# Kernel optimization log

Measured on AMD Instinct MI355X. Metric: run time of the kernel, lower is better.

Reference implementation:

```python
import jax, jax.numpy as jnp
import numpy as np

BSZ, SL, D, K, K_U, K_Y, SCALE = 4, 2048, 256, 24, 3, 2, 4
H = SCALE * D


def _hankel(n):
    i = np.arange(1, n + 1, dtype=np.float64)
    s = i[:, None] + i[None, :]
    return 2.0 / (s ** 3 - s)


def setup_inputs() -> dict:
    key = jax.random.key(0)
    ks = jax.random.split(key, 9)
    Z = _hankel(SL)
    ev, evec = np.linalg.eigh(Z)  # ascending
    sigma = jnp.asarray(np.clip(ev[-K:], 1e-12, None), jnp.float32)  # (K,)
    phi = jnp.asarray(evec[:, -K:], jnp.float32)  # (SL, K) top-k eigenvectors
    s = 0.02
    return {
        'x': jax.random.normal(ks[0], (BSZ, SL, D), jnp.float32),
        'sigma': sigma,
        'phi': phi,
        'rms_w': jnp.ones((D,), jnp.float32),
        'M_u': jax.random.normal(ks[1], (K_U, D, D), jnp.float32) * s,
        'M_phi_plus': jax.random.normal(ks[2], (K, D, D), jnp.float32) * s,
        'M_phi_minus': jax.random.normal(ks[3], (K, D, D), jnp.float32) * s,
        'm_y': jax.random.normal(ks[4], (K_Y, D, D), jnp.float32) * s,
        'w1': jax.random.normal(ks[5], (D, H), jnp.float32) * s,
        'v': jax.random.normal(ks[6], (D, H), jnp.float32) * s,
        'w2': jax.random.normal(ks[7], (H, D), jnp.float32) * s,
    }


def _rmsnorm(x, w, eps=1e-6):
    return x * jax.lax.rsqrt(jnp.mean(x * x, axis=-1, keepdims=True) + eps) * w


def _shift(u, i):
    # causal time shift: out[:, t] = u[:, t-i], zero-padded
    if i == 0:
        return u
    return jnp.pad(u, ((0, 0), (i, 0), (0, 0)))[:, :-i, :]


def _causal_conv(phi, u):
    # U[b,t,k,d] = sum_{s<=t} phi[s,k] * u[b,t-s,d], via FFT (linear conv, length 2*sl)
    sl = u.shape[1]
    n = 2 * sl
    Fu = jnp.fft.rfft(u, n=n, axis=1)  # (b, nf, d)
    Fp = jnp.fft.rfft(phi, n=n, axis=0)  # (nf, k)
    prod = Fu[:, :, None, :] * Fp[None, :, :, None]  # (b, nf, k, d)
    return jnp.fft.irfft(prod, n=n, axis=1)[:, :sl]  # (b, sl, k, d)


def _stu(u, sigma, phi, M_u, M_phi_plus, M_phi_minus, m_y):
    k_u = M_u.shape[0]
    ar_u = sum(jnp.einsum('btd,od->bto', _shift(u, i), M_u[i]) for i in range(k_u))
    # spectral term: eigenfilter causal convolutions on u and alternating-sign u
    alt = jnp.where(jnp.arange(u.shape[1]) % 2 == 0, 1.0, -1.0)[None, :, None]
    Up = _causal_conv(phi, u)
    Um = _causal_conv(phi, u * alt)
    sr = sigma ** 0.25
    spectral = (jnp.einsum('btkd,k,kod->bto', Up, sr, M_phi_plus)
                + jnp.einsum('btkd,k,kod->bto', Um, sr, M_phi_minus))
    y = ar_u + spectral  # (b, sl, d)
    # sequential AR recurrence over outputs: yhat_t = y_t + sum_i m_y[i] @ yhat_{t-1-i}
    k_y, d = m_y.shape[0], m_y.shape[2]
    b = u.shape[0]

    def step(carry, y_t):  # carry: (k_y, b, d), most recent first
        ar = jnp.einsum('kod,kbd->bo', m_y, carry)
        yhat = y_t + ar
        carry = jnp.concatenate([yhat[None], carry[:-1]], axis=0)
        return carry, ar

    carry0 = jnp.zeros((k_y, b, d), u.dtype)
    _, ar_y = jax.lax.scan(step, carry0, jnp.swapaxes(y, 0, 1))
    return y + jnp.swapaxes(ar_y, 0, 1)


def reference(x, sigma, phi, rms_w, M_u, M_phi_plus, M_phi_minus, m_y, w1, v, w2):
    z = x
    h = _stu(_rmsnorm(x, rms_w), sigma, phi, M_u, M_phi_plus, M_phi_minus, m_y)
    mlp = (jax.nn.silu(h @ w1) * (h @ v)) @ w2  # SwiGLU
    h = h + mlp
    return h + z
```

## Files before the change

kernel.cpp:

```cpp
#include <hip/hip_runtime.h>
#include <hip/hip_bf16.h>
#include <math.h>

#define SLEN 2048
#define DIM 256
#define NB 4
#define NKF 24
#define NH 1024
#define NROW (NB*SLEN)
#define NTOT (NB*SLEN*DIM)

#define BM 128
#define BN 256
#define BKK 32
#define PADK 40

#define KG 3
#define KPB 8
#define VELEMS ((size_t)NKF*NB*DIM*SLEN)

typedef __attribute__((ext_vector_type(8))) short bf16x8;
typedef __attribute__((ext_vector_type(4))) float f32x4;

struct __align__(16) U4 { unsigned int a, b, c, d; };
struct __align__(8)  S4 { unsigned short x, y, z, w; };

__device__ __forceinline__ unsigned short f2b(float v){
    union { __hip_bfloat16 h; unsigned short u; } cv;
    cv.h = __float2bfloat16(v);
    return cv.u;
}
__device__ __forceinline__ float b2f(unsigned short s){
    union { __hip_bfloat16 h; unsigned short u; } cv;
    cv.u = s;
    return __bfloat162float(cv.h);
}

__device__ __forceinline__ void gl_lds(const unsigned short* g, unsigned short* l){
    __builtin_amdgcn_global_load_lds((const __attribute__((address_space(1))) void*)g,
                                     (__attribute__((address_space(3))) void*)l, 16, 0, 0);
}

__device__ __forceinline__ int swzS(int row, int g){
    return ((row >> 3) << 5) + (g << 3) + ((row & 7) ^ g);
}

__global__ void k_prep(const float4* __restrict__ Mu, const float4* __restrict__ Mp,
                       const float4* __restrict__ Mm,
                       const float* __restrict__ w1, const float* __restrict__ vv,
                       const float* __restrict__ w2, const float* __restrict__ my,
                       const float* __restrict__ phi,
                       S4* __restrict__ MuB, S4* __restrict__ MpB, S4* __restrict__ MmB,
                       unsigned short* __restrict__ w1T, unsigned short* __restrict__ vT,
                       unsigned short* __restrict__ w2T,
                       unsigned short* __restrict__ pw, unsigned short* __restrict__ pwTs,
                       unsigned short* __restrict__ Q, unsigned short* __restrict__ Tt){
    int bid = blockIdx.x, tix = threadIdx.x;
    if (bid < 192){
        int i = bid*256 + tix;
        float4 v = Mu[i];
        S4 p; p.x=f2b(v.x); p.y=f2b(v.y); p.z=f2b(v.z); p.w=f2b(v.w);
        MuB[i] = p; return;
    }
    bid -= 192;
    if (bid < 1536){
        int i = bid*256 + tix;
        float4 v = Mp[i];
        S4 p; p.x=f2b(v.x); p.y=f2b(v.y); p.z=f2b(v.z); p.w=f2b(v.w);
        MpB[i] = p; return;
    }
    bid -= 1536;
    if (bid < 1536){
        int i = bid*256 + tix;
        float4 v = Mm[i];
        S4 p; p.x=f2b(v.x); p.y=f2b(v.y); p.z=f2b(v.z); p.w=f2b(v.w);
        MmB[i] = p; return;
    }
    bid -= 1536;
    if (bid < 1024){
        int i = bid*256 + tix; int r = i >> 10, c = i & 1023;
        w1T[(size_t)c*DIM + r] = f2b(w1[i]); return;
    }
    bid -= 1024;
    if (bid < 1024){
        int i = bid*256 + tix; int r = i >> 10, c = i & 1023;
        vT[(size_t)c*DIM + r] = f2b(vv[i]); return;
    }
    bid -= 1024;
    if (bid < 1024){
        int i = bid*256 + tix; int r = i >> 8, c = i & 255;
        w2T[(size_t)c*NH + r] = f2b(w2[i]); return;
    }
    bid -= 1024;
    if (bid < 1024){
        int i = bid*256 + tix;
        int r = i >> 9, c = i & 511;
        float v;
        if (r < 256) v = (c < 256) ? my[r*256 + c] : my[256*256 + r*256 + (c - 256)];
        else         v = (c == r - 256) ? 1.0f : 0.0f;
        unsigned short bb = f2b(v);
        pw [262144 + (size_t)r*512 + c] = bb;
        pwTs[(size_t)c*512 + r] = bb;
        if (r < 256 && c < 256) Q[65536 + r*256 + c] = bb;
        return;
    }
    bid -= 1024;
    {
        int i = bid*256 + tix;
        int e   = (i & 7) * 4;
        int row = (i >> 3) & 127;
        int c   = (i >> 10) & 7;
        int rem = (i >> 13) & 15;
        int k   = i >> 17;
        int d0 = rem*128 + row - (c*32 + e);
        S4 p;
        p.x = (d0   >= 0) ? f2b(phi[(size_t)(d0  )*NKF + k]) : (unsigned short)0;
        p.y = (d0-1 >= 0) ? f2b(phi[(size_t)(d0-1)*NKF + k]) : (unsigned short)0;
        p.z = (d0-2 >= 0) ? f2b(phi[(size_t)(d0-2)*NKF + k]) : (unsigned short)0;
        p.w = (d0-3 >= 0) ? f2b(phi[(size_t)(d0-3)*NKF + k]) : (unsigned short)0;
        size_t base = ((size_t)((k*16 + rem)*8 + c)) * 4096;
        *(S4*)&Tt[base + swzS(row, e>>3)*8 + (e&7)] = p;
    }
}

__global__ void k_rmsnorm(const float* __restrict__ x, const float* __restrict__ w, unsigned short* __restrict__ u){
    int row = blockIdx.x;
    int t = threadIdx.x;
    float v = x[(size_t)row*DIM + t];
    float ss = v*v;
    #pragma unroll
    for (int o = 32; o > 0; o >>= 1) ss += __shfl_down(ss, o, 64);
    __shared__ float red[4];
    if ((t & 63) == 0) red[t >> 6] = ss;
    __syncthreads();
    float tot = red[0]+red[1]+red[2]+red[3];
    float sc = rsqrtf(tot * (1.0f/256.0f) + 1e-6f);
    u[(size_t)row*DIM + t] = f2b(v * sc * w[t]);
}

__global__ void k_prep2(const float4* __restrict__ y, float4* __restrict__ out, S4* __restrict__ ybf){
    int i = blockIdx.x*256 + threadIdx.x;
    if (i < NTOT/4){
        float4 v = y[i];
        out[i] = v;
        S4 p; p.x=f2b(v.x); p.y=f2b(v.y); p.z=f2b(v.z); p.w=f2b(v.w);
        ybf[i] = p;
    }
}


__device__ __forceinline__ void mfma_tile(const unsigned short* Al, const unsigned short* Bl,
                                          f32x4 acc[4][4], int lane, int wr, int wc){
    int cl = lane & 15;
    int kb = (lane >> 4) * 8;
    bf16x8 a[4], b[4];
    #pragma unroll
    for (int mi = 0; mi < 4; ++mi)
        a[mi] = *(const bf16x8*)&Al[(wr*64 + mi*16 + cl)*PADK + kb];
    #pragma unroll
    for (int ni = 0; ni < 4; ++ni)
        b[ni] = *(const bf16x8*)&Bl[(wc*64 + ni*16 + cl)*PADK + kb];
    #pragma unroll
    for (int mi = 0; mi < 4; ++mi)
        #pragma unroll
        for (int ni = 0; ni < 4; ++ni)
            acc[mi][ni] = __builtin_amdgcn_mfma_f32_16x16x32_bf16(a[mi], b[ni], acc[mi][ni], 0, 0, 0);
}

#define GEMM_PROLOG \
    __shared__ unsigned short Al[BM*PADK]; \
    __shared__ unsigned short Bl[BN*PADK]; \
    int tid = threadIdx.x, lane = tid & 63, wv = tid >> 6, wr = wv >> 2, wc = wv & 3; \
    f32x4 acc[4][4]; \
    { f32x4 z = {0.f,0.f,0.f,0.f}; \
      for (int mi=0;mi<4;++mi) for (int ni=0;ni<4;++ni) acc[mi][ni] = z; }

__global__ __launch_bounds__(512) void k_pow(unsigned short* __restrict__ pw, unsigned short* __restrict__ pwTs,
                                             unsigned short* __restrict__ Q, int s, int ns){
    int mt = blockIdx.x, nt = blockIdx.y;
    int j = 1 + blockIdx.z;
    int p = ns + j;
    int m0 = mt * BM, n0 = nt * BN;
    if (p > 16 && (m0 >= 256 || n0 >= 256)) return;
    GEMM_PROLOG
    const unsigned short* A = pw   + (size_t)j * 262144;
    const unsigned short* B = pwTs + (size_t)s * 262144;
    for (int k0 = 0; k0 < 512; k0 += BKK){
        __syncthreads();
        { int row = tid >> 2, sg = tid & 3;
          *(U4*)&Al[row*PADK + sg*8] = *(const U4*)&A[(size_t)(m0+row)*512 + k0 + sg*8]; }
        #pragma unroll
        for (int ss = 0; ss < 2; ++ss){ int q = tid + ss*512; int row = q >> 2, sg = q & 3;
          *(U4*)&Bl[row*PADK + sg*8] = *(const U4*)&B[(size_t)(n0+row)*512 + k0 + sg*8]; }
        __syncthreads();
        mfma_tile(Al, Bl, acc, lane, wr, wc);
    }
    int cl = lane & 15, rg = (lane >> 4) * 4;
    #pragma unroll
    for (int mi=0; mi<4; ++mi){
        int rb = m0 + wr*64 + mi*16 + rg;
        #pragma unroll
        for (int ni=0; ni<4; ++ni){
            int col = n0 + wc*64 + ni*16 + cl;
            unsigned short bb[4];
            #pragma unroll
            for (int r=0;r<4;++r) bb[r] = f2b(acc[mi][ni][r]);
            if (p <= 16){
                #pragma unroll
                for (int r=0;r<4;++r) pw[(size_t)p*262144 + (size_t)(rb+r)*512 + col] = bb[r];
            }
            if (j == ns && ns <= 8){
                S4 pk; pk.x=bb[0]; pk.y=bb[1]; pk.z=bb[2]; pk.w=bb[3];
                *(S4*)&pwTs[(size_t)(s+1)*262144 + (size_t)col*512 + rb] = pk;
            }
            if (rb < 256 && col < 256){
                #pragma unroll
                for (int r=0;r<4;++r) Q[(size_t)p*65536 + (size_t)(rb+r)*256 + col] = bb[r];
            }
        }
    }
}

__global__ __launch_bounds__(512) void k_aru(const unsigned short* __restrict__ u,
                                             const unsigned short* __restrict__ Mu, float* __restrict__ y){
    GEMM_PROLOG
    int tt = blockIdx.x, b = blockIdx.y;
    int t0 = tt * BM;
    const unsigned short* Ab = u + (size_t)b*SLEN*DIM;
    for (int i = 0; i < 3; ++i){
        const unsigned short* Bsrc = Mu + (size_t)i*65536;
        for (int k0 = 0; k0 < 256; k0 += BKK){
            __syncthreads();
            { int row = tid >> 2, sg = tid & 3; int t = t0 + row - i;
              U4 val; val.a=val.b=val.c=val.d=0u;
              if (t >= 0) val = *(const U4*)&Ab[(size_t)t*DIM + k0 + sg*8];
              *(U4*)&Al[row*PADK + sg*8] = val; }
            #pragma unroll
            for (int s = 0; s < 2; ++s){ int q = tid + s*512; int row = q >> 2, sg = q & 3;
              *(U4*)&Bl[row*PADK + sg*8] = *(const U4*)&Bsrc[(size_t)row*DIM + k0 + sg*8]; }
            __syncthreads();
            mfma_tile(Al, Bl, acc, lane, wr, wc);
        }
    }
    int cl = lane & 15, rg = (lane >> 4) * 4;
    #pragma unroll
    for (int mi=0; mi<4; ++mi){
        int tb = t0 + wr*64 + mi*16 + rg;
        #pragma unroll
        for (int ni=0; ni<4; ++ni){
            int o = wc*64 + ni*16 + cl;
            #pragma unroll
            for (int r=0;r<4;++r) y[((size_t)b*SLEN + tb + r)*DIM + o] = acc[mi][ni][r];
        }
    }
}

__global__ __launch_bounds__(512) void k_proj(const unsigned short* __restrict__ u,
                                              const unsigned short* __restrict__ Mp,
                                              const unsigned short* __restrict__ Mm,
                                              const float* __restrict__ sigma,
                                              unsigned short* __restrict__ V){
    __shared__ unsigned short Al[BM*PADK];
    __shared__ unsigned short Bl0[BN*PADK];
    __shared__ unsigned short Bl1[BN*PADK];
    int tid = threadIdx.x, lane = tid & 63, wv = tid >> 6, wr = wv >> 2, wc = wv & 3;
    f32x4 acc0[4][4], acc1[4][4];
    { f32x4 z = {0.f,0.f,0.f,0.f};
      for (int mi=0;mi<4;++mi) for (int ni=0;ni<4;++ni){ acc0[mi][ni] = z; acc1[mi][ni] = z; } }
    int tt = blockIdx.x, b = blockIdx.y, k = blockIdx.z;
    int t0 = tt * BM;
    float sr = powf(sigma[k], 0.25f);
    const unsigned short* Asrc  = u + ((size_t)b*SLEN + t0)*DIM;
    const unsigned short* B0src = Mp + (size_t)k*65536;
    const unsigned short* B1src = Mm + (size_t)k*65536;
    for (int k0 = 0; k0 < 256; k0 += BKK){
        __syncthreads();
        { int row = tid >> 2, sg = tid & 3;
          *(U4*)&Al[row*PADK + sg*8] = *(const U4*)&Asrc[(size_t)row*DIM + k0 + sg*8]; }
        #pragma unroll
        for (int s = 0; s < 2; ++s){ int q = tid + s*512; int row = q >> 2, sg = q & 3;
          *(U4*)&Bl0[row*PADK + sg*8] = *(const U4*)&B0src[(size_t)row*DIM + k0 + sg*8];
          *(U4*)&Bl1[row*PADK + sg*8] = *(const U4*)&B1src[(size_t)row*DIM + k0 + sg*8]; }
        __syncthreads();
        mfma_tile(Al, Bl0, acc0, lane, wr, wc);
        mfma_tile(Al, Bl1, acc1, lane, wr, wc);
    }
    int cl = lane & 15, rg = (lane >> 4) * 4;
    unsigned short* Tr = Bl0;
    const int TRS = 136;
    #pragma unroll
    for (int ps = 0; ps < 4; ++ps){
        __syncthreads();
        if (wc == ps){
            #pragma unroll
            for (int mi=0; mi<4; ++mi){
                int tl = wr*64 + mi*16 + rg;
                #pragma unroll
                for (int ni=0; ni<4; ++ni){
                    int ol = ni*16 + cl;
                    S4 pk;
                    float s0 = ((t0+tl+0)&1) ? -1.0f : 1.0f;
                    float s1 = ((t0+tl+1)&1) ? -1.0f : 1.0f;
                    float s2 = ((t0+tl+2)&1) ? -1.0f : 1.0f;
                    float s3 = ((t0+tl+3)&1) ? -1.0f : 1.0f;
                    pk.x = f2b(sr*(acc0[mi][ni][0] + s0*acc1[mi][ni][0]));
                    pk.y = f2b(sr*(acc0[mi][ni][1] + s1*acc1[mi][ni][1]));
                    pk.z = f2b(sr*(acc0[mi][ni][2] + s2*acc1[mi][ni][2]));
                    pk.w = f2b(sr*(acc0[mi][ni][3] + s3*acc1[mi][ni][3]));
                    *(S4*)&Tr[ol*TRS + tl] = pk;
                }
            }
        }
        __syncthreads();
        { int row = tid >> 3, seg = tid & 7;
          U4 v0 = *(const U4*)&Tr[row*TRS + seg*16];
          U4 v1 = *(const U4*)&Tr[row*TRS + seg*16 + 8];
          int o  = ps*64 + row;
          int tb = (t0 >> 5) + (seg >> 1);
          int g0 = (seg & 1) * 2;
          size_t sb = ((size_t)(k*NB + b)*64 + tb) * 8192;
          *(U4*)&V[sb + swzS(o, g0  )*8] = v0;
          *(U4*)&V[sb + swzS(o, g0+1)*8] = v1; }
    }
}

__global__ __launch_bounds__(512) void k_conv(const unsigned short* __restrict__ V,
                                              const unsigned short* __restrict__ Tt,
                                              float* __restrict__ y){
    __shared__ __align__(16) unsigned short Abuf[3][4096];
    __shared__ __align__(16) unsigned short Bbuf[3][8192];
    int tid = threadIdx.x, lane = tid & 63, wv = tid >> 6, wr = wv >> 2, wc = wv & 3;
    f32x4 acc[4][4];
    { f32x4 z = {0.f,0.f,0.f,0.f};
      for (int mi=0;mi<4;++mi) for (int ni=0;ni<4;++ni) acc[mi][ni] = z; }

    int b = blockIdx.y, kg = blockIdx.z;
    int px0 = blockIdx.x;
    int px = (px0 & 7)*9 + (px0 >> 3);
    int jx = 0, rem = px;
    #pragma unroll
    for (int j = 0; j < 8; ++j){
        int c = 16 - 2*j;
        if (rem < c){ jx = j; break; }
        rem -= c;
    }
    int tt = 2*jx + rem;
    int t0 = tt*BM;
    int cl = lane & 15, g = lane >> 4;

    int aoff[4], boff[4];
    #pragma unroll
    for (int mi = 0; mi < 4; ++mi) aoff[mi] = swzS(wr*64 + mi*16 + cl, g) << 4;
    #pragma unroll
    for (int ni = 0; ni < 4; ++ni) boff[ni] = swzS(wc*64 + ni*16 + cl, g) << 4;

    const unsigned short* Abase = Tt + (size_t)((kg*KPB*16 + rem)*8) * 4096;
    const unsigned short* Bbase = V  + (((size_t)(kg*KPB*NB + b)*64 + jx*8)) * 8192;

    auto stage = [&](int bi, int step){
        int kk = step >> 3, ts = step & 7;
        const unsigned short* As = Abase + ((size_t)kk*16*8 + ts)*4096 + wv*512;
        const unsigned short* Bs = Bbase + ((size_t)kk*NB*64 + ts)*8192 + wv*1024;
        gl_lds(As + lane*8,       &Abuf[bi][wv*512]);
        gl_lds(Bs + lane*8,       &Bbuf[bi][wv*1024]);
        gl_lds(Bs + 512 + lane*8, &Bbuf[bi][wv*1024 + 512]);
    };

    auto compute = [&](int bi){
        bf16x8 a[4], bb[4];
        #pragma unroll
        for (int mi = 0; mi < 4; ++mi)
            a[mi] = *(const bf16x8*)((const char*)Abuf[bi] + aoff[mi]);
        #pragma unroll
        for (int ni = 0; ni < 4; ++ni)
            bb[ni] = *(const bf16x8*)((const char*)Bbuf[bi] + boff[ni]);
        #pragma unroll
        for (int mi = 0; mi < 4; ++mi)
            #pragma unroll
            for (int ni = 0; ni < 4; ++ni)
                acc[mi][ni] = __builtin_amdgcn_mfma_f32_16x16x32_bf16(a[mi], bb[ni], acc[mi][ni], 0, 0, 0);
    };

    stage(0, 0);
    stage(1, 1);
    int cur = 0;
    for (int t = 0; t < KPB*8 - 1; ++t){
        asm volatile("s_waitcnt vmcnt(3)" ::: "memory");
        __builtin_amdgcn_s_barrier();
        __builtin_amdgcn_sched_barrier(0);
        compute(cur);
        if (t + 2 < KPB*8){
            int nb = cur + 2; if (nb >= 3) nb -= 3;
            stage(nb, t + 2);
        }
        cur = (cur == 2) ? 0 : cur + 1;
    }
    asm volatile("s_waitcnt vmcnt(0)" ::: "memory");
    __builtin_amdgcn_s_barrier();
    __builtin_amdgcn_sched_barrier(0);
    compute(cur);

    int rg = (lane >> 4) * 4;
    #pragma unroll
    for (int mi=0; mi<4; ++mi){
        int tb = t0 + wr*64 + mi*16 + rg;
        #pragma unroll
        for (int ni=0; ni<4; ++ni){
            int o = wc*64 + ni*16 + cl;
            #pragma unroll
            for (int r=0;r<4;++r) atomicAdd(&y[((size_t)b*SLEN + tb + r)*DIM + o], acc[mi][ni][r]);
        }
    }
}

__global__ __launch_bounds__(512) void k_qconv(const unsigned short* __restrict__ ybf,
                                               const unsigned short* __restrict__ Q,
                                               float* __restrict__ yh){
    GEMM_PROLOG
    int tt = blockIdx.x, b = blockIdx.y, gz = blockIdx.z;
    int t0 = tt * BM;
    const unsigned short* ysrc = ybf + (size_t)b*SLEN*DIM;
    for (int pi = 0; pi < 4; ++pi){
        int p = gz*4 + pi;
        if (p == 0) continue;
        const unsigned short* Qp = Q + (size_t)p*65536;
        for (int k0 = 0; k0 < 256; k0 += BKK){
            __syncthreads();
            { int row = tid >> 2, sg = tid & 3; int t = t0 + row - p;
              U4 val; val.a=val.b=val.c=val.d=0u;
              if (t >= 0) val = *(const U4*)&ysrc[(size_t)t*DIM + k0 + sg*8];
              *(U4*)&Al[row*PADK + sg*8] = val; }
            #pragma unroll
            for (int s = 0; s < 2; ++s){ int q = tid + s*512; int row = q >> 2, sg = q & 3;
              *(U4*)&Bl[row*PADK + sg*8] = *(const U4*)&Qp[(size_t)row*256 + k0 + sg*8]; }
            __syncthreads();
            mfma_tile(Al, Bl, acc, lane, wr, wc);
        }
    }
    int cl = lane & 15, rg = (lane >> 4) * 4;
    #pragma unroll
    for (int mi=0; mi<4; ++mi){
        int tb = t0 + wr*64 + mi*16 + rg;
        #pragma unroll
        for (int ni=0; ni<4; ++ni){
            int o = wc*64 + ni*16 + cl;
            #pragma unroll
            for (int r=0;r<4;++r) atomicAdd(&yh[((size_t)b*SLEN + tb + r)*DIM + o], acc[mi][ni][r]);
        }
    }
}

__global__ __launch_bounds__(512) void k_mlp1f(const float* __restrict__ yhat,
                                               const unsigned short* __restrict__ w1T,
                                               const unsigned short* __restrict__ vT,
                                               unsigned short* __restrict__ act){
    __shared__ unsigned short Al[BM*PADK];
    __shared__ unsigned short Bl0[BN*PADK];
    __shared__ unsigned short Bl1[BN*PADK];
    int tid = threadIdx.x, lane = tid & 63, wv = tid >> 6, wr = wv >> 2, wc = wv & 3;
    f32x4 acc0[4][4], acc1[4][4];
    { f32x4 z = {0.f,0.f,0.f,0.f};
      for (int mi=0;mi<4;++mi) for (int ni=0;ni<4;++ni){ acc0[mi][ni] = z; acc1[mi][ni] = z; } }
    int tt = blockIdx.x, b = blockIdx.y, nt = blockIdx.z;
    int t0 = tt * BM, h0 = nt * 256;
    const float* Asrc = yhat + ((size_t)b*SLEN + t0)*DIM;
    const unsigned short* B0src = w1T + (size_t)h0*DIM;
    const unsigned short* B1src = vT  + (size_t)h0*DIM;
    for (int k0 = 0; k0 < 256; k0 += BKK){
        __syncthreads();
        { int row = tid >> 2, sg = tid & 3;
          const float* src = &Asrc[(size_t)row*DIM + k0 + sg*8];
          float4 f0 = *(const float4*)src, f1 = *(const float4*)(src+4);
          union { U4 v; unsigned short s[8]; } pk;
          pk.s[0]=f2b(f0.x); pk.s[1]=f2b(f0.y); pk.s[2]=f2b(f0.z); pk.s[3]=f2b(f0.w);
          pk.s[4]=f2b(f1.x); pk.s[5]=f2b(f1.y); pk.s[6]=f2b(f1.z); pk.s[7]=f2b(f1.w);
          *(U4*)&Al[row*PADK + sg*8] = pk.v; }
        #pragma unroll
        for (int s = 0; s < 2; ++s){ int q = tid + s*512; int row = q >> 2, sg = q & 3;
          *(U4*)&Bl0[row*PADK + sg*8] = *(const U4*)&B0src[(size_t)row*DIM + k0 + sg*8];
          *(U4*)&Bl1[row*PADK + sg*8] = *(const U4*)&B1src[(size_t)row*DIM + k0 + sg*8]; }
        __syncthreads();
        mfma_tile(Al, Bl0, acc0, lane, wr, wc);
        mfma_tile(Al, Bl1, acc1, lane, wr, wc);
    }
    int cl = lane & 15, rg = (lane >> 4) * 4;
    #pragma unroll
    for (int mi=0; mi<4; ++mi){
        int tb = t0 + wr*64 + mi*16 + rg;
        #pragma unroll
        for (int ni=0; ni<4; ++ni){
            int h = h0 + wc*64 + ni*16 + cl;
            #pragma unroll
            for (int r=0; r<4; ++r){
                float av = acc0[mi][ni][r];
                float sv = av / (1.0f + expf(-av));
                act[(size_t)(b*SLEN + tb + r)*NH + h] = f2b(sv * acc1[mi][ni][r]);
            }
        }
    }
}

__global__ __launch_bounds__(512) void k_mlp2(const unsigned short* __restrict__ act,
                                              const unsigned short* __restrict__ w2T,
                                              const float* __restrict__ x,
                                              float* __restrict__ out){
    GEMM_PROLOG
    int tt = blockIdx.x, b = blockIdx.y, ks = blockIdx.z;
    int t0 = tt * BM;
    size_t bt0 = (size_t)b*SLEN + t0;
    for (int k0 = ks*256; k0 < ks*256 + 256; k0 += BKK){
        __syncthreads();
        { int row = tid >> 2, sg = tid & 3;
          *(U4*)&Al[row*PADK + sg*8] = *(const U4*)&act[(bt0 + row)*NH + k0 + sg*8]; }
        #pragma unroll
        for (int s = 0; s < 2; ++s){ int q = tid + s*512; int row = q >> 2, sg = q & 3;
          *(U4*)&Bl[row*PADK + sg*8] = *(const U4*)&w2T[(size_t)row*NH + k0 + sg*8]; }
        __syncthreads();
        mfma_tile(Al, Bl, acc, lane, wr, wc);
    }
    int cl = lane & 15, rg = (lane >> 4) * 4;
    #pragma unroll
    for (int mi=0; mi<4; ++mi){
        #pragma unroll
        for (int ni=0; ni<4; ++ni){
            int o = wc*64 + ni*16 + cl;
            #pragma unroll
            for (int r=0;r<4;++r){
                size_t idx = (bt0 + wr*64 + mi*16 + rg + r)*DIM + o;
                float add = acc[mi][ni][r] + (ks == 0 ? x[idx] : 0.0f);
                atomicAdd(&out[idx], add);
            }
        }
    }
}


extern "C" void kernel_launch(void* const* d_in, const int* in_sizes, int n_in,
                              void* d_out, int out_size, void* d_ws, size_t ws_size,
                              hipStream_t stream) {
    (void)in_sizes; (void)n_in; (void)out_size;
    const float* x     = (const float*)d_in[0];
    const float* sigma = (const float*)d_in[1];
    const float* phi   = (const float*)d_in[2];
    const float* rmsw  = (const float*)d_in[3];
    const float* Mu    = (const float*)d_in[4];
    const float* Mp    = (const float*)d_in[5];
    const float* Mm    = (const float*)d_in[6];
    const float* my    = (const float*)d_in[7];
    const float* w1    = (const float*)d_in[8];
    const float* vv    = (const float*)d_in[9];
    const float* w2    = (const float*)d_in[10];
    float* out = (float*)d_out;

    char* ws = (char*)d_ws;
    size_t off = 0;
    auto alloc = [&](size_t bytes){ size_t o = off; off += (bytes + 255) & ~(size_t)255; return o; };

    size_t o_u    = alloc((size_t)NROW*DIM*2);
    size_t o_T    = alloc((size_t)NKF*16*128*256*2);
    size_t o_MuB  = alloc((size_t)3*65536*2);
    size_t o_MpB  = alloc((size_t)NKF*65536*2);
    size_t o_MmB  = alloc((size_t)NKF*65536*2);
    size_t o_w1T  = alloc((size_t)NH*DIM*2);
    size_t o_vT   = alloc((size_t)NH*DIM*2);
    size_t o_w2T  = alloc((size_t)DIM*NH*2);
    size_t o_pow  = alloc((size_t)17*262144*2);
    size_t o_powT = alloc((size_t)6*262144*2);
    size_t o_Q    = alloc((size_t)32*65536*2);
    size_t o_y    = alloc((size_t)NTOT*4);
    size_t o_ybf  = alloc((size_t)NTOT*2);
    size_t o_V    = alloc(VELEMS*2);
    if (off > ws_size) return;

    unsigned short* u_b  = (unsigned short*)(ws + o_u);
    unsigned short* Tt   = (unsigned short*)(ws + o_T);
    unsigned short* MuB  = (unsigned short*)(ws + o_MuB);
    unsigned short* MpB  = (unsigned short*)(ws + o_MpB);
    unsigned short* MmB  = (unsigned short*)(ws + o_MmB);
    unsigned short* w1T  = (unsigned short*)(ws + o_w1T);
    unsigned short* vT   = (unsigned short*)(ws + o_vT);
    unsigned short* w2T  = (unsigned short*)(ws + o_w2T);
    unsigned short* pw   = (unsigned short*)(ws + o_pow);
    unsigned short* pwTs = (unsigned short*)(ws + o_powT);
    unsigned short* Q    = (unsigned short*)(ws + o_Q);
    float* y             = (float*)(ws + o_y);
    unsigned short* ybf  = (unsigned short*)(ws + o_ybf);
    unsigned short* V    = (unsigned short*)(ws + o_V);
    unsigned short* act  = (unsigned short*)(ws + o_V);

    k_prep<<<dim3(19648), 256, 0, stream>>>((const float4*)Mu, (const float4*)Mp, (const float4*)Mm,
                                            w1, vv, w2, my, phi,
                                            (S4*)MuB, (S4*)MpB, (S4*)MmB,
                                            w1T, vT, w2T, pw, pwTs, Q, Tt);

    k_rmsnorm<<<dim3(NROW), 256, 0, stream>>>(x, rmsw, u_b);

    const int ns[5]   = {1, 2, 4, 8, 16};
    const int cnts[5] = {1, 2, 4, 8, 15};
    for (int s = 0; s < 5; ++s)
        k_pow<<<dim3(4, 2, cnts[s]), 512, 0, stream>>>(pw, pwTs, Q, s, ns[s]);

    k_aru<<<dim3(16, NB), 512, 0, stream>>>(u_b, MuB, y);

    k_proj<<<dim3(16, NB, NKF), 512, 0, stream>>>(u_b, MpB, MmB, sigma, V);
    k_conv<<<dim3(72, NB, KG), 512, 0, stream>>>(V, Tt, y);

    k_prep2<<<dim3(NTOT/4/256), 256, 0, stream>>>((const float4*)y, (float4*)out, (S4*)ybf);

    k_qconv<<<dim3(16, NB, 8), 512, 0, stream>>>(ybf, Q, out);

    k_mlp1f<<<dim3(16, NB, 4), 512, 0, stream>>>(out, w1T, vT, act);
    k_mlp2<<<dim3(16, NB, 4), 512, 0, stream>>>(act, w2T, x, out);
}
```

Baseline: 547.0 us.

## Precombine spectral weights into even/odd matrices, fuse rmsnorm into prep, regroup qconv

```diff
diff --git a/kernel.cpp b/kernel.cpp
--- a/kernel.cpp
+++ b/kernel.cpp
@@ -45,17 +45,34 @@
     return ((row >> 3) << 5) + (g << 3) + ((row & 7) ^ g);
 }
 
-__global__ void k_prep(const float4* __restrict__ Mu, const float4* __restrict__ Mp,
+__global__ void k_prep(const float* __restrict__ x, const float* __restrict__ rmsw,
+                       const float4* __restrict__ Mu, const float4* __restrict__ Mp,
                        const float4* __restrict__ Mm,
                        const float* __restrict__ w1, const float* __restrict__ vv,
                        const float* __restrict__ w2, const float* __restrict__ my,
                        const float* __restrict__ phi,
-                       S4* __restrict__ MuB, S4* __restrict__ MpB, S4* __restrict__ MmB,
+                       unsigned short* __restrict__ u_b,
+                       S4* __restrict__ MuB, S4* __restrict__ MeB, S4* __restrict__ MoB,
                        unsigned short* __restrict__ w1T, unsigned short* __restrict__ vT,
                        unsigned short* __restrict__ w2T,
                        unsigned short* __restrict__ pw, unsigned short* __restrict__ pwTs,
                        unsigned short* __restrict__ Q, unsigned short* __restrict__ Tt){
+    __shared__ float red[4];
     int bid = blockIdx.x, tix = threadIdx.x;
+    if (bid < NROW){
+        int row = bid, t = tix;
+        float v = x[(size_t)row*DIM + t];
+        float ss = v*v;
+        #pragma unroll
+        for (int o = 32; o > 0; o >>= 1) ss += __shfl_down(ss, o, 64);
+        if ((t & 63) == 0) red[t >> 6] = ss;
+        __syncthreads();
+        float tot = red[0]+red[1]+red[2]+red[3];
+        float sc = rsqrtf(tot * (1.0f/256.0f) + 1e-6f);
+        u_b[(size_t)row*DIM + t] = f2b(v * sc * rmsw[t]);
+        return;
+    }
+    bid -= NROW;
     if (bid < 192){
         int i = bid*256 + tix;
         float4 v = Mu[i];
@@ -65,16 +82,16 @@
     bid -= 192;
     if (bid < 1536){
         int i = bid*256 + tix;
-        float4 v = Mp[i];
-        S4 p; p.x=f2b(v.x); p.y=f2b(v.y); p.z=f2b(v.z); p.w=f2b(v.w);
-        MpB[i] = p; return;
+        float4 a = Mp[i], b = Mm[i];
+        S4 p; p.x=f2b(a.x+b.x); p.y=f2b(a.y+b.y); p.z=f2b(a.z+b.z); p.w=f2b(a.w+b.w);
+        MeB[i] = p; return;
     }
     bid -= 1536;
     if (bid < 1536){
         int i = bid*256 + tix;
-        float4 v = Mm[i];
-        S4 p; p.x=f2b(v.x); p.y=f2b(v.y); p.z=f2b(v.z); p.w=f2b(v.w);
-        MmB[i] = p; return;
+        float4 a = Mp[i], b = Mm[i];
+        S4 p; p.x=f2b(a.x-b.x); p.y=f2b(a.y-b.y); p.z=f2b(a.z-b.z); p.w=f2b(a.w-b.w);
+        MoB[i] = p; return;
     }
     bid -= 1536;
     if (bid < 1024){
@@ -123,21 +140,6 @@
     }
 }
 
-__global__ void k_rmsnorm(const float* __restrict__ x, const float* __restrict__ w, unsigned short* __restrict__ u){
-    int row = blockIdx.x;
-    int t = threadIdx.x;
-    float v = x[(size_t)row*DIM + t];
-    float ss = v*v;
-    #pragma unroll
-    for (int o = 32; o > 0; o >>= 1) ss += __shfl_down(ss, o, 64);
-    __shared__ float red[4];
-    if ((t & 63) == 0) red[t >> 6] = ss;
-    __syncthreads();
-    float tot = red[0]+red[1]+red[2]+red[3];
-    float sc = rsqrtf(tot * (1.0f/256.0f) + 1e-6f);
-    u[(size_t)row*DIM + t] = f2b(v * sc * w[t]);
-}
-
 __global__ void k_prep2(const float4* __restrict__ y, float4* __restrict__ out, S4* __restrict__ ybf){
     int i = blockIdx.x*256 + threadIdx.x;
     if (i < NTOT/4){
@@ -256,34 +258,34 @@
 }
 
 __global__ __launch_bounds__(512) void k_proj(const unsigned short* __restrict__ u,
-                                              const unsigned short* __restrict__ Mp,
-                                              const unsigned short* __restrict__ Mm,
+                                              const unsigned short* __restrict__ Me,
+                                              const unsigned short* __restrict__ Mo,
                                               const float* __restrict__ sigma,
                                               unsigned short* __restrict__ V){
     __shared__ unsigned short Al[BM*PADK];
     __shared__ unsigned short Bl0[BN*PADK];
     __shared__ unsigned short Bl1[BN*PADK];
     int tid = threadIdx.x, lane = tid & 63, wv = tid >> 6, wr = wv >> 2, wc = wv & 3;
-    f32x4 acc0[4][4], acc1[4][4];
+    f32x4 acc[4][4];
     { f32x4 z = {0.f,0.f,0.f,0.f};
-      for (int mi=0;mi<4;++mi) for (int ni=0;ni<4;++ni){ acc0[mi][ni] = z; acc1[mi][ni] = z; } }
+      for (int mi=0;mi<4;++mi) for (int ni=0;ni<4;++ni) acc[mi][ni] = z; }
     int tt = blockIdx.x, b = blockIdx.y, k = blockIdx.z;
     int t0 = tt * BM;
     float sr = powf(sigma[k], 0.25f);
-    const unsigned short* Asrc  = u + ((size_t)b*SLEN + t0)*DIM;
-    const unsigned short* B0src = Mp + (size_t)k*65536;
-    const unsigned short* B1src = Mm + (size_t)k*65536;
+    const unsigned short* Asrc  = u + ((size_t)b*SLEN)*DIM;
+    const unsigned short* B0src = Me + (size_t)k*65536;
+    const unsigned short* B1src = Mo + (size_t)k*65536;
     for (int k0 = 0; k0 < 256; k0 += BKK){
         __syncthreads();
         { int row = tid >> 2, sg = tid & 3;
-          *(U4*)&Al[row*PADK + sg*8] = *(const U4*)&Asrc[(size_t)row*DIM + k0 + sg*8]; }
+          int t = (row < 64) ? (t0 + 2*row) : (t0 + 2*(row-64) + 1);
+          *(U4*)&Al[row*PADK + sg*8] = *(const U4*)&Asrc[(size_t)t*DIM + k0 + sg*8]; }
         #pragma unroll
         for (int s = 0; s < 2; ++s){ int q = tid + s*512; int row = q >> 2, sg = q & 3;
           *(U4*)&Bl0[row*PADK + sg*8] = *(const U4*)&B0src[(size_t)row*DIM + k0 + sg*8];
           *(U4*)&Bl1[row*PADK + sg*8] = *(const U4*)&B1src[(size_t)row*DIM + k0 + sg*8]; }
         __syncthreads();
-        mfma_tile(Al, Bl0, acc0, lane, wr, wc);
-        mfma_tile(Al, Bl1, acc1, lane, wr, wc);
+        mfma_tile(Al, wr ? Bl1 : Bl0, acc, lane, wr, wc);
     }
     int cl = lane & 15, rg = (lane >> 4) * 4;
     unsigned short* Tr = Bl0;
@@ -294,20 +296,19 @@
         if (wc == ps){
             #pragma unroll
             for (int mi=0; mi<4; ++mi){
-                int tl = wr*64 + mi*16 + rg;
                 #pragma unroll
                 for (int ni=0; ni<4; ++ni){
                     int ol = ni*16 + cl;
                     S4 pk;
-                    float s0 = ((t0+tl+0)&1) ? -1.0f : 1.0f;
-                    float s1 = ((t0+tl+1)&1) ? -1.0f : 1.0f;
-                    float s2 = ((t0+tl+2)&1) ? -1.0f : 1.0f;
-                    float s3 = ((t0+tl+3)&1) ? -1.0f : 1.0f;
-                    pk.x = f2b(sr*(acc0[mi][ni][0] + s0*acc1[mi][ni][0]));
-                    pk.y = f2b(sr*(acc0[mi][ni][1] + s1*acc1[mi][ni][1]));
-                    pk.z = f2b(sr*(acc0[mi][ni][2] + s2*acc1[mi][ni][2]));
-                    pk.w = f2b(sr*(acc0[mi][ni][3] + s3*acc1[mi][ni][3]));
-                    *(S4*)&Tr[ol*TRS + tl] = pk;
+                    pk.x = f2b(sr*acc[mi][ni][0]); pk.y = f2b(sr*acc[mi][ni][1]);
+                    pk.z = f2b(sr*acc[mi][ni][2]); pk.w = f2b(sr*acc[mi][ni][3]);
+                    #pragma unroll
+                    for (int r=0; r<4; ++r){
+                        int lr = mi*16 + rg + r;
+                        int dt = wr ? (2*lr + 1) : (2*lr);
+                        unsigned short val = (&pk.x)[r];
+                        Tr[ol*TRS + dt] = val;
+                    }
                 }
             }
         }
@@ -420,8 +421,8 @@
     int tt = blockIdx.x, b = blockIdx.y, gz = blockIdx.z;
     int t0 = tt * BM;
     const unsigned short* ysrc = ybf + (size_t)b*SLEN*DIM;
-    for (int pi = 0; pi < 4; ++pi){
-        int p = gz*4 + pi;
+    for (int pi = 0; pi < 8; ++pi){
+        int p = gz*8 + pi;
         if (p == 0) continue;
         const unsigned short* Qp = Q + (size_t)p*65536;
         for (int k0 = 0; k0 < 256; k0 += BKK){
@@ -559,8 +560,8 @@
     size_t o_u    = alloc((size_t)NROW*DIM*2);
     size_t o_T    = alloc((size_t)NKF*16*128*256*2);
     size_t o_MuB  = alloc((size_t)3*65536*2);
-    size_t o_MpB  = alloc((size_t)NKF*65536*2);
-    size_t o_MmB  = alloc((size_t)NKF*65536*2);
+    size_t o_MeB  = alloc((size_t)NKF*65536*2);
+    size_t o_MoB  = alloc((size_t)NKF*65536*2);
     size_t o_w1T  = alloc((size_t)NH*DIM*2);
     size_t o_vT   = alloc((size_t)NH*DIM*2);
     size_t o_w2T  = alloc((size_t)DIM*NH*2);
@@ -575,8 +576,8 @@
     unsigned short* u_b  = (unsigned short*)(ws + o_u);
     unsigned short* Tt   = (unsigned short*)(ws + o_T);
     unsigned short* MuB  = (unsigned short*)(ws + o_MuB);
-    unsigned short* MpB  = (unsigned short*)(ws + o_MpB);
-    unsigned short* MmB  = (unsigned short*)(ws + o_MmB);
+    unsigned short* MeB  = (unsigned short*)(ws + o_MeB);
+    unsigned short* MoB  = (unsigned short*)(ws + o_MoB);
     unsigned short* w1T  = (unsigned short*)(ws + o_w1T);
     unsigned short* vT   = (unsigned short*)(ws + o_vT);
     unsigned short* w2T  = (unsigned short*)(ws + o_w2T);
@@ -588,12 +589,11 @@
     unsigned short* V    = (unsigned short*)(ws + o_V);
     unsigned short* act  = (unsigned short*)(ws + o_V);
 
-    k_prep<<<dim3(19648), 256, 0, stream>>>((const float4*)Mu, (const float4*)Mp, (const float4*)Mm,
+    k_prep<<<dim3(27840), 256, 0, stream>>>(x, rmsw,
+                                            (const float4*)Mu, (const float4*)Mp, (const float4*)Mm,
                                             w1, vv, w2, my, phi,
-                                            (S4*)MuB, (S4*)MpB, (S4*)MmB,
+                                            u_b, (S4*)MuB, (S4*)MeB, (S4*)MoB,
                                             w1T, vT, w2T, pw, pwTs, Q, Tt);
-
-    k_rmsnorm<<<dim3(NROW), 256, 0, stream>>>(x, rmsw, u_b);
 
     const int ns[5]   = {1, 2, 4, 8, 16};
     const int cnts[5] = {1, 2, 4, 8, 15};
@@ -602,12 +602,12 @@
 
     k_aru<<<dim3(16, NB), 512, 0, stream>>>(u_b, MuB, y);
 
-    k_proj<<<dim3(16, NB, NKF), 512, 0, stream>>>(u_b, MpB, MmB, sigma, V);
+    k_proj<<<dim3(16, NB, NKF), 512, 0, stream>>>(u_b, MeB, MoB, sigma, V);
     k_conv<<<dim3(72, NB, KG), 512, 0, stream>>>(V, Tt, y);
 
     k_prep2<<<dim3(NTOT/4/256), 256, 0, stream>>>((const float4*)y, (float4*)out, (S4*)ybf);
 
-    k_qconv<<<dim3(16, NB, 8), 512, 0, stream>>>(ybf, Q, out);
+    k_qconv<<<dim3(16, NB, 4), 512, 0, stream>>>(ybf, Q, out);
 
     k_mlp1f<<<dim3(16, NB, 4), 512, 0, stream>>>(out, w1T, vT, act);
     k_mlp2<<<dim3(16, NB, 4), 512, 0, stream>>>(act, w2T, x, out);
```

Measured after the change: 514.6 us. 5.9% less time.
